# Kernel optimization log

Measured on AMD Instinct MI355X. Metric: run time of the kernel, lower is better.

Reference implementation:

```python
import jax, jax.numpy as jnp
import numpy as np

NUM_SAMPLED = 8192
NUM_TRUE = 1


def setup_inputs() -> dict:
    key = jax.random.key(0)
    k1, k2, k3 = jax.random.split(key, 3)
    B, D, V = 16384, 128, 1000000
    return {
        "movie_id_tensor": jax.random.normal(k1, (B, D), dtype=jnp.float32),
        "target_movie_ids": jax.random.randint(k2, (B, NUM_TRUE), 0, V, dtype=jnp.int64),
        "embedding": jax.random.normal(k3, (V, D), dtype=jnp.float32),
        "bias": jnp.zeros((V,), dtype=jnp.float32),
    }


def _log_uniform_logprob(ids, log_range):
    # log-uniform (Zipf) sampler probability: P(c) = (log(c+2)-log(c+1)) / log(V+1)
    idsf = ids.astype(jnp.float32)
    return jnp.log((jnp.log(idsf + 2.0) - jnp.log(idsf + 1.0)) / log_range)


def reference(movie_id_tensor, target_movie_ids, embedding, bias):
    V, D = embedding.shape
    log_range = jnp.log(jnp.float32(V + 1))
    # --- draw num_sampled candidates from the log-uniform distribution ---
    u = jax.random.uniform(jax.random.key(1), (NUM_SAMPLED,), dtype=jnp.float32)
    sampled = jnp.clip(
        jnp.floor(jnp.exp(u * log_range)).astype(jnp.int32) - 1, 0, V - 1
    )  # [S]
    log_ns = jnp.log(jnp.float32(NUM_SAMPLED))
    # --- gather true-class rows and compute true logits (with logQ correction) ---
    true_w = embedding[target_movie_ids]                  # [B, T, D]
    true_b = bias[target_movie_ids]                       # [B, T]
    true_logits = (
        jnp.einsum("bd,btd->bt", movie_id_tensor, true_w)
        + true_b
        - (log_ns + _log_uniform_logprob(target_movie_ids, log_range))
    )                                                     # [B, T]
    # --- sampled logits (shared candidate set across the batch) ---
    sampled_w = embedding[sampled]                        # [S, D]
    sampled_b = bias[sampled]                             # [S]
    sampled_logits = (
        movie_id_tensor @ sampled_w.T
        + sampled_b
        - (log_ns + _log_uniform_logprob(sampled, log_range))
    )                                                     # [B, S]
    # --- remove accidental hits (sampled id equals a true label) ---
    hit = (sampled[None, None, :] == target_movie_ids[:, :, None]).any(axis=1)  # [B, S]
    sampled_logits = jnp.where(hit, sampled_logits - 1e9, sampled_logits)
    # --- softmax CE with labels = 1/num_true on the true columns ---
    logits = jnp.concatenate([true_logits, sampled_logits], axis=1)  # [B, T+S]
    loss = jax.nn.logsumexp(logits, axis=1) - true_logits.sum(axis=1) / NUM_TRUE
    return loss  # [B]
```

## Files before the change

### kernel.cpp

```cpp
#include <hip/hip_runtime.h>
#include <math.h>

#define BB      16384
#define DD      128
#define VV      1000000
#define NSAMP   8192
#define NT      (NSAMP / 64)

typedef __attribute__((ext_vector_type(8)))  unsigned short u16x8;
typedef __attribute__((ext_vector_type(8)))  __bf16         bf16x8;
typedef __attribute__((ext_vector_type(16))) float          f32x16;

__device__ __forceinline__ unsigned rotl32(unsigned x, unsigned r) {
    return (x << r) | (x >> (32u - r));
}

__device__ __forceinline__ unsigned short bf16r(float v) {
    unsigned b = __builtin_bit_cast(unsigned, v);
    unsigned r = (b + 0x7fffu + ((b >> 16) & 1u)) >> 16;
    return (unsigned short)r;
}

__device__ __forceinline__ void gload16(const void* g, void* l) {
    __builtin_amdgcn_global_load_lds(
        (const __attribute__((address_space(1))) unsigned*)g,
        (__attribute__((address_space(3))) unsigned*)l, 16, 0, 0);
}

__device__ __forceinline__ float xla_expf(float x) {
#pragma clang fp contract(off)
    float fx = floorf(x * 1.44269504088896341f + 0.5f);
    float tmp = fx * 0.693359375f;
    float z2  = fx * -2.12194440e-4f;
    float r = x - tmp;
    r = r - z2;
    float z = r * r;
    float y = 1.9875691500E-4f;
    y = y * r + 1.3981999507E-3f;
    y = y * r + 8.3334519073E-3f;
    y = y * r + 4.1665795894E-2f;
    y = y * r + 1.6666665459E-1f;
    y = y * r + 5.0000001201E-1f;
    y = y * z + r;
    y = y + 1.0f;
    int n = (int)fx;
    float p2n = __builtin_bit_cast(float, (unsigned)((n + 127) << 23));
    return y * p2n;
}

__device__ __forceinline__ float log_q32(float idf, float logr) {
    float l2 = (float)log((double)(idf + 2.0f));
    float l1 = (float)log((double)(idf + 1.0f));
    float q  = (l2 - l1) / logr;
    return (float)log((double)q);
}

__global__ __launch_bounds__(256) void prep_kernel(
    const float* __restrict__ x, const unsigned* __restrict__ tgt_raw,
    const float* __restrict__ bias,
    unsigned short* __restrict__ Xb,
    int* __restrict__ ids, float* __restrict__ corr,
    unsigned* __restrict__ flag, float logr, float logns)
{
    if (blockIdx.x == 0) {
        __shared__ unsigned red[256];
        unsigned acc = 0;
        for (int i = threadIdx.x; i < 2048; i += 256) acc |= tgt_raw[2 * i + 1];
        red[threadIdx.x] = acc;
        __syncthreads();
        for (int s = 128; s > 0; s >>= 1) {
            if ((int)threadIdx.x < s) red[threadIdx.x] |= red[threadIdx.x + s];
            __syncthreads();
        }
        if (threadIdx.x == 0) flag[0] = (red[0] == 0u) ? 1u : 0u;
    }

    int g = blockIdx.x * 256 + threadIdx.x;
    {
        int row = g >> 4, chunk = g & 15;
        const float4* src = (const float4*)(x + (size_t)row * DD + chunk * 8);
        float4 a = src[0], b = src[1];
        uint4 o;
        o.x = (unsigned)bf16r(a.x) | ((unsigned)bf16r(a.y) << 16);
        o.y = (unsigned)bf16r(a.z) | ((unsigned)bf16r(a.w) << 16);
        o.z = (unsigned)bf16r(b.x) | ((unsigned)bf16r(b.y) << 16);
        o.w = (unsigned)bf16r(b.z) | ((unsigned)bf16r(b.w) << 16);
        *(uint4*)(Xb + (size_t)row * DD + chunk * 8) = o;
    }

    if (g < NSAMP) {
        int i = g;
        const unsigned k0 = 0u, k1 = 1u;
        const unsigned k2 = 0x1BD11BDAu ^ k0 ^ k1;
        unsigned x0 = 0u + k0;
        unsigned x1 = (unsigned)i + k1;
#define TFR(r) { x0 += x1; x1 = rotl32(x1, (r)); x1 ^= x0; }
        TFR(13) TFR(15) TFR(26) TFR(6)   x0 += k1; x1 += k2 + 1u;
        TFR(17) TFR(29) TFR(16) TFR(24)  x0 += k2; x1 += k0 + 2u;
        TFR(13) TFR(15) TFR(26) TFR(6)   x0 += k0; x1 += k1 + 3u;
        TFR(17) TFR(29) TFR(16) TFR(24)  x0 += k1; x1 += k2 + 4u;
        TFR(13) TFR(15) TFR(26) TFR(6)   x0 += k2; x1 += k0 + 5u;
#undef TFR
        unsigned bits = x0 ^ x1;

        unsigned fb = (bits >> 9) | 0x3f800000u;
        float u = __builtin_bit_cast(float, fb) - 1.0f;
        float t = u * logr;
        float ef = xla_expf(t);
        int id = (int)floorf(ef) - 1;
        id = id < 0 ? 0 : (id > VV - 1 ? VV - 1 : id);

        float lp = log_q32((float)id, logr);
        ids[i]  = id;
        corr[i] = bias[id] - (logns + lp);
    }
}

__global__ __launch_bounds__(256) void gather_kernel(
    const float* __restrict__ emb, const int* __restrict__ ids,
    unsigned short* __restrict__ Wh)
{
    int g = blockIdx.x * 256 + threadIdx.x;
    int row   = g >> 4;
    int chunk = g & 15;
    const float4* src = (const float4*)(emb + (size_t)ids[row] * DD + chunk * 8);
    float4 a = src[0], b = src[1];
    uint4 o;
    o.x = (unsigned)bf16r(a.x) | ((unsigned)bf16r(a.y) << 16);
    o.y = (unsigned)bf16r(a.z) | ((unsigned)bf16r(a.w) << 16);
    o.z = (unsigned)bf16r(b.x) | ((unsigned)bf16r(b.y) << 16);
    o.w = (unsigned)bf16r(b.z) | ((unsigned)bf16r(b.w) << 16);
    *(uint4*)(Wh + (size_t)row * DD + chunk * 8) = o;
}

__device__ __forceinline__ int swz(int row, int slot) {
    return row * 256 + ((slot ^ (row & 15)) << 4);
}

__global__ __launch_bounds__(256, 2) void gemm_kernel(
    const unsigned short* __restrict__ Xb, const int* __restrict__ tgt,
    const unsigned* __restrict__ flag,
    const unsigned short* __restrict__ Wh,
    const int* __restrict__ ids, const float* __restrict__ corr,
    float* __restrict__ ps)
{
    __shared__ char lds[32768];

    const int tid  = threadIdx.x;
    const int lane = tid & 63;
    const int wid  = tid >> 6;
    const int wr   = wid >> 1, wc = wid & 1;
    const int half = lane >> 5, ln31 = lane & 31;
    const int m0   = blockIdx.x * 128;
    const int ty0  = blockIdx.y * (NT / 4);

    u16x8 ah[2][8];
    #pragma unroll
    for (int p = 0; p < 2; p++) {
        const uint4* xr = (const uint4*)(Xb + (size_t)(m0 + wr * 64 + p * 32 + ln31) * DD);
        #pragma unroll
        for (int ks = 0; ks < 8; ks++)
            ah[p][ks] = __builtin_bit_cast(u16x8, xr[ks * 2 + half]);
    }

    const unsigned is64 = flag[0];
    int t32[2][16];
    #pragma unroll
    for (int p = 0; p < 2; p++)
        #pragma unroll
        for (int i = 0; i < 16; i++) {
            int grow = m0 + wr * 64 + p * 32 + (i & 3) + 8 * (i >> 2) + 4 * half;
            t32[p][i] = is64 ? tgt[2 * grow] : tgt[grow];
        }

    float ss[2][16];
    #pragma unroll
    for (int p = 0; p < 2; p++)
        #pragma unroll
        for (int i = 0; i < 16; i++) ss[p][i] = 0.f;

    const int u    = lane & 15;
    const int rsub = lane >> 4;
    int srcoff[4], ldsrow[4];
    #pragma unroll
    for (int i2 = 0; i2 < 4; i2++) {
        int row = wid * 16 + i2 * 4 + rsub;
        srcoff[i2] = row * 256 + ((u ^ (row & 15)) << 4);
        ldsrow[i2] = (wid * 16 + i2 * 4) * 256;
    }
    const int brow = wc * 32 + ln31;

    {
        const char* tb = (const char*)Wh + (size_t)(ty0 * 64) * 256;
        #pragma unroll
        for (int i2 = 0; i2 < 4; i2++)
            gload16(tb + srcoff[i2], lds + ldsrow[i2]);
    }
    __syncthreads();

    for (int t = 0; t < NT / 4; t++) {
        const int c = t & 1;
        if (t + 1 < NT / 4) {
            const char* tb = (const char*)Wh + (size_t)((ty0 + t + 1) * 64) * 256;
            char* db = lds + (c ^ 1) * 16384;
            #pragma unroll
            for (int i2 = 0; i2 < 4; i2++)
                gload16(tb + srcoff[i2], db + ldsrow[i2]);
        }

        const char* bh_base = lds + c * 16384;
        f32x16 h0, h1;
        #pragma unroll
        for (int q = 0; q < 16; q++) { h0[q] = 0.f; h1[q] = 0.f; }

        #pragma unroll
        for (int ks = 0; ks < 8; ks++) {
            int off = swz(brow, ks * 2 + half);
            bf16x8 bh = __builtin_bit_cast(bf16x8, *(const uint4*)(bh_base + off));
            bf16x8 a0 = __builtin_bit_cast(bf16x8, ah[0][ks]);
            bf16x8 a1 = __builtin_bit_cast(bf16x8, ah[1][ks]);
            h0 = __builtin_amdgcn_mfma_f32_32x32x16_bf16(a0, bh, h0, 0, 0, 0);
            h1 = __builtin_amdgcn_mfma_f32_32x32x16_bf16(a1, bh, h1, 0, 0, 0);
        }

        const int j = (ty0 + t) * 64 + wc * 32 + ln31;
        const float cc = corr[j] - 60.0f;
        const int idj = ids[j];
        #pragma unroll
        for (int i = 0; i < 16; i++) {
            float l0 = h0[i] + cc;
            float l1 = h1[i] + cc;
            ss[0][i] += (idj == t32[0][i]) ? 0.0f : __expf(l0);
            ss[1][i] += (idj == t32[1][i]) ? 0.0f : __expf(l1);
        }

        __syncthreads();
    }

    #pragma unroll
    for (int p = 0; p < 2; p++)
        #pragma unroll
        for (int i = 0; i < 16; i++) {
            float v = ss[p][i];
            v += __shfl_xor(v, 1);
            v += __shfl_xor(v, 2);
            v += __shfl_xor(v, 4);
            v += __shfl_xor(v, 8);
            v += __shfl_xor(v, 16);
            if (ln31 == 0) {
                int grow = m0 + wr * 64 + p * 32 + (i & 3) + 8 * (i >> 2) + 4 * half;
                ps[(size_t)grow * 8 + blockIdx.y * 2 + wc] = v;
            }
        }
}

__global__ __launch_bounds__(256) void finish_kernel(
    const float* __restrict__ x, const int* __restrict__ tgt,
    const float* __restrict__ emb, const float* __restrict__ bias,
    const unsigned* __restrict__ flag, const float* __restrict__ ps,
    float* __restrict__ out, float logr, float logns)
{
    const int gid = blockIdx.x * 256 + threadIdx.x;
    const int r   = gid >> 4;
    const int l   = gid & 15;
    if (r >= BB) return;

    const int t = flag[0] ? tgt[2 * r] : tgt[r];

    const float4* xr = (const float4*)(x + (size_t)r * DD);
    const float4* wr = (const float4*)(emb + (size_t)t * DD);
    float4 xa = xr[l], xb = xr[l + 16];
    float4 wa = wr[l], wb = wr[l + 16];
    float d = xa.x*wa.x + xa.y*wa.y + xa.z*wa.z + xa.w*wa.w
            + xb.x*wb.x + xb.y*wb.y + xb.z*wb.z + xb.w*wb.w;
    d += __shfl_xor(d, 1);
    d += __shfl_xor(d, 2);
    d += __shfl_xor(d, 4);
    d += __shfl_xor(d, 8);

    if (l == 0) {
        float lp = log_q32((float)t, logr);
        float tl = d + bias[t] - (logns + lp);
        const float* p = ps + (size_t)r * 8;
        float S = ((p[0] + p[1]) + (p[2] + p[3])) + ((p[4] + p[5]) + (p[6] + p[7]));
        out[r] = logf(expf(tl - 60.0f) + S) + 60.0f - tl;
    }
}

extern "C" void kernel_launch(void* const* d_in, const int* in_sizes, int n_in,
                              void* d_out, int out_size, void* d_ws, size_t ws_size,
                              hipStream_t stream)
{
    const float* x    = (const float*)d_in[0];
    const int*   tgt  = (const int*)d_in[1];
    const float* emb  = (const float*)d_in[2];
    const float* bias = (const float*)d_in[3];
    float* out = (float*)d_out;

    char* w = (char*)d_ws;
    int*            ids  = (int*)(w + 0);
    float*          corr = (float*)(w + 32768);
    unsigned*       flag = (unsigned*)(w + 65536);
    unsigned short* Xb   = (unsigned short*)(w + 131072);
    unsigned short* Wh   = (unsigned short*)(w + 131072 + 4194304);
    float*          ps   = (float*)(w + 131072 + 4194304 + 2097152);

    const float logr  = (float)log(1000001.0);
    const float logns = (float)log(8192.0);

    prep_kernel<<<dim3(BB * 16 / 256), dim3(256), 0, stream>>>(
        x, (const unsigned*)tgt, bias, Xb, ids, corr, flag, logr, logns);
    gather_kernel<<<dim3(NSAMP * 16 / 256), dim3(256), 0, stream>>>(
        emb, ids, Wh);
    gemm_kernel<<<dim3(BB / 128, 4), dim3(256), 0, stream>>>(
        Xb, tgt, flag, Wh, ids, corr, ps);
    finish_kernel<<<dim3(BB * 16 / 256), dim3(256), 0, stream>>>(
        x, tgt, emb, bias, flag, ps, out, logr, logns);
}
```

Measured before the change: 75.05 us.

## Split sampled columns 8 ways, raise occupancy, precompute int32 targets in prep

```diff
diff --git a/kernel.cpp b/kernel.cpp
--- a/kernel.cpp
+++ b/kernel.cpp
@@ -56,28 +56,35 @@
 }
 
 __global__ __launch_bounds__(256) void prep_kernel(
-    const float* __restrict__ x, const unsigned* __restrict__ tgt_raw,
+    const float* __restrict__ x, const int* __restrict__ tgt,
     const float* __restrict__ bias,
-    unsigned short* __restrict__ Xb,
+    unsigned short* __restrict__ Xb, int* __restrict__ tgt32,
     int* __restrict__ ids, float* __restrict__ corr,
-    unsigned* __restrict__ flag, float logr, float logns)
-{
-    if (blockIdx.x == 0) {
-        __shared__ unsigned red[256];
+    float logr, float logns)
+{
+    __shared__ unsigned red[256];
+    __shared__ unsigned is64s;
+    {
+        const unsigned* traw = (const unsigned*)tgt;
         unsigned acc = 0;
-        for (int i = threadIdx.x; i < 2048; i += 256) acc |= tgt_raw[2 * i + 1];
+        for (int i = threadIdx.x; i < 2048; i += 256) acc |= traw[2 * i + 1];
         red[threadIdx.x] = acc;
         __syncthreads();
         for (int s = 128; s > 0; s >>= 1) {
             if ((int)threadIdx.x < s) red[threadIdx.x] |= red[threadIdx.x + s];
             __syncthreads();
         }
-        if (threadIdx.x == 0) flag[0] = (red[0] == 0u) ? 1u : 0u;
-    }
+        if (threadIdx.x == 0) is64s = (red[0] == 0u) ? 1u : 0u;
+        __syncthreads();
+    }
+    const unsigned is64 = is64s;
 
     int g = blockIdx.x * 256 + threadIdx.x;
+    int row = g >> 4, chunk = g & 15;
+
+    if (chunk == 0) tgt32[row] = is64 ? tgt[2 * row] : tgt[row];
+
     {
-        int row = g >> 4, chunk = g & 15;
         const float4* src = (const float4*)(x + (size_t)row * DD + chunk * 8);
         float4 a = src[0], b = src[1];
         uint4 o;
@@ -137,9 +144,8 @@
     return row * 256 + ((slot ^ (row & 15)) << 4);
 }
 
-__global__ __launch_bounds__(256, 2) void gemm_kernel(
-    const unsigned short* __restrict__ Xb, const int* __restrict__ tgt,
-    const unsigned* __restrict__ flag,
+__global__ __launch_bounds__(256, 4) void gemm_kernel(
+    const unsigned short* __restrict__ Xb, const int* __restrict__ tgt32,
     const unsigned short* __restrict__ Wh,
     const int* __restrict__ ids, const float* __restrict__ corr,
     float* __restrict__ ps)
@@ -152,7 +158,8 @@
     const int wr   = wid >> 1, wc = wid & 1;
     const int half = lane >> 5, ln31 = lane & 31;
     const int m0   = blockIdx.x * 128;
-    const int ty0  = blockIdx.y * (NT / 4);
+    const int ty0  = blockIdx.y * (NT / 8);
+    const int NTB  = NT / 8;
 
     u16x8 ah[2][8];
     #pragma unroll
@@ -162,16 +169,6 @@
         for (int ks = 0; ks < 8; ks++)
             ah[p][ks] = __builtin_bit_cast(u16x8, xr[ks * 2 + half]);
     }
-
-    const unsigned is64 = flag[0];
-    int t32[2][16];
-    #pragma unroll
-    for (int p = 0; p < 2; p++)
-        #pragma unroll
-        for (int i = 0; i < 16; i++) {
-            int grow = m0 + wr * 64 + p * 32 + (i & 3) + 8 * (i >> 2) + 4 * half;
-            t32[p][i] = is64 ? tgt[2 * grow] : tgt[grow];
-        }
 
     float ss[2][16];
     #pragma unroll
@@ -189,6 +186,7 @@
         ldsrow[i2] = (wid * 16 + i2 * 4) * 256;
     }
     const int brow = wc * 32 + ln31;
+    const int tb0  = m0 + wr * 64;
 
     {
         const char* tb = (const char*)Wh + (size_t)(ty0 * 64) * 256;
@@ -198,9 +196,9 @@
     }
     __syncthreads();
 
-    for (int t = 0; t < NT / 4; t++) {
+    for (int t = 0; t < NTB; t++) {
         const int c = t & 1;
-        if (t + 1 < NT / 4) {
+        if (t + 1 < NTB) {
             const char* tb = (const char*)Wh + (size_t)((ty0 + t + 1) * 64) * 256;
             char* db = lds + (c ^ 1) * 16384;
             #pragma unroll
@@ -228,10 +226,17 @@
         const int idj = ids[j];
         #pragma unroll
         for (int i = 0; i < 16; i++) {
+            const int ro = (i & 3) + 8 * (i >> 2);
+            int tA0 = tgt32[tb0 + ro];
+            int tA1 = tgt32[tb0 + ro + 4];
+            int tB0 = tgt32[tb0 + 32 + ro];
+            int tB1 = tgt32[tb0 + 32 + ro + 4];
+            int ttA = half ? tA1 : tA0;
+            int ttB = half ? tB1 : tB0;
             float l0 = h0[i] + cc;
             float l1 = h1[i] + cc;
-            ss[0][i] += (idj == t32[0][i]) ? 0.0f : __expf(l0);
-            ss[1][i] += (idj == t32[1][i]) ? 0.0f : __expf(l1);
+            ss[0][i] += (idj == ttA) ? 0.0f : __expf(l0);
+            ss[1][i] += (idj == ttB) ? 0.0f : __expf(l1);
         }
 
         __syncthreads();
@@ -249,15 +254,15 @@
             v += __shfl_xor(v, 16);
             if (ln31 == 0) {
                 int grow = m0 + wr * 64 + p * 32 + (i & 3) + 8 * (i >> 2) + 4 * half;
-                ps[(size_t)grow * 8 + blockIdx.y * 2 + wc] = v;
+                ps[(size_t)grow * 16 + blockIdx.y * 2 + wc] = v;
             }
         }
 }
 
 __global__ __launch_bounds__(256) void finish_kernel(
-    const float* __restrict__ x, const int* __restrict__ tgt,
+    const float* __restrict__ x, const int* __restrict__ tgt32,
     const float* __restrict__ emb, const float* __restrict__ bias,
-    const unsigned* __restrict__ flag, const float* __restrict__ ps,
+    const float* __restrict__ ps,
     float* __restrict__ out, float logr, float logns)
 {
     const int gid = blockIdx.x * 256 + threadIdx.x;
@@ -265,7 +270,7 @@
     const int l   = gid & 15;
     if (r >= BB) return;
 
-    const int t = flag[0] ? tgt[2 * r] : tgt[r];
+    const int t = tgt32[r];
 
     const float4* xr = (const float4*)(x + (size_t)r * DD);
     const float4* wr = (const float4*)(emb + (size_t)t * DD);
@@ -281,8 +286,10 @@
     if (l == 0) {
         float lp = log_q32((float)t, logr);
         float tl = d + bias[t] - (logns + lp);
-        const float* p = ps + (size_t)r * 8;
-        float S = ((p[0] + p[1]) + (p[2] + p[3])) + ((p[4] + p[5]) + (p[6] + p[7]));
+        const float* p = ps + (size_t)r * 16;
+        float S = 0.f;
+        #pragma unroll
+        for (int k = 0; k < 16; k++) S += p[k];
         out[r] = logf(expf(tl - 60.0f) + S) + 60.0f - tl;
     }
 }
@@ -298,22 +305,22 @@
     float* out = (float*)d_out;
 
     char* w = (char*)d_ws;
-    int*            ids  = (int*)(w + 0);
-    float*          corr = (float*)(w + 32768);
-    unsigned*       flag = (unsigned*)(w + 65536);
-    unsigned short* Xb   = (unsigned short*)(w + 131072);
-    unsigned short* Wh   = (unsigned short*)(w + 131072 + 4194304);
-    float*          ps   = (float*)(w + 131072 + 4194304 + 2097152);
+    int*            ids   = (int*)(w + 0);
+    float*          corr  = (float*)(w + 32768);
+    int*            tgt32 = (int*)(w + 65536);
+    unsigned short* Xb    = (unsigned short*)(w + 131072);
+    unsigned short* Wh    = (unsigned short*)(w + 131072 + 4194304);
+    float*          ps    = (float*)(w + 131072 + 4194304 + 2097152);
 
     const float logr  = (float)log(1000001.0);
     const float logns = (float)log(8192.0);
 
     prep_kernel<<<dim3(BB * 16 / 256), dim3(256), 0, stream>>>(
-        x, (const unsigned*)tgt, bias, Xb, ids, corr, flag, logr, logns);
+        x, tgt, bias, Xb, tgt32, ids, corr, logr, logns);
     gather_kernel<<<dim3(NSAMP * 16 / 256), dim3(256), 0, stream>>>(
         emb, ids, Wh);
-    gemm_kernel<<<dim3(BB / 128, 4), dim3(256), 0, stream>>>(
-        Xb, tgt, flag, Wh, ids, corr, ps);
+    gemm_kernel<<<dim3(BB / 128, 8), dim3(256), 0, stream>>>(
+        Xb, tgt32, Wh, ids, corr, ps);
     finish_kernel<<<dim3(BB * 16 / 256), dim3(256), 0, stream>>>(
-        x, tgt, emb, bias, flag, ps, out, logr, logns);
-}
+        x, tgt32, emb, bias, ps, out, logr, logns);
+}
```

Result: slower. 194.0 us (+158.5%).
